# Optimization experiments

Hardware: AMD Instinct MI355X
Metric: run time of the kernel (lower is better)

Reference implementation:

```python
import jax, jax.numpy as jnp
import numpy as np

B, NB, DIM = 4096, 64, 256
CNT_R = 500
CNT_E = CNT_R * 2  # padding relation id == CNT_E maps to the masked row
N_WR = CNT_R * 2 + 1
N_ZQ = CNT_R * 2


def setup_inputs() -> dict:
    key = jax.random.key(0)
    ks = jax.random.split(key, 10)
    batch_nei_rid = jax.random.randint(ks[0], (B, NB), 0, N_WR, dtype=jnp.int64 if jax.config.read('jax_enable_x64') else jnp.int32)
    batch_nei_e_emb = jax.random.normal(ks[1], (B, NB, DIM), dtype=jnp.float32)
    batch_nei_rw = jax.random.uniform(ks[2], (B, NB), dtype=jnp.float32)
    batch_q_rid = jax.random.randint(ks[3], (B,), 0, N_ZQ, dtype=jnp.int32)
    # xavier-normal-ish params
    def xav(k, shape):
        fan_in, fan_out = shape[-1], shape[-2] if len(shape) > 1 else shape[-1]
        std = (2.0 / (fan_in + fan_out)) ** 0.5
        return (jax.random.normal(k, shape) * std).astype(jnp.float32)
    w_r_weight = xav(ks[4], (N_WR, DIM))
    zq_weight = xav(ks[5], (N_ZQ, DIM))
    attn_W_w = xav(ks[6], (2 * DIM, 2 * DIM))   # [out, in], torch Linear layout
    attn_W_b = jnp.zeros((2 * DIM,), jnp.float32)
    u_a_w = xav(ks[7], (1, 2 * DIM))
    u_a_b = jnp.zeros((1,), jnp.float32)
    return {
        'batch_nei_rid': batch_nei_rid,
        'batch_nei_e_emb': batch_nei_e_emb,
        'batch_nei_rw': batch_nei_rw,
        'batch_q_rid': batch_q_rid,
        'w_r_weight': w_r_weight,
        'zq_weight': zq_weight,
        'attn_W_w': attn_W_w,
        'attn_W_b': attn_W_b,
        'u_a_w': u_a_w,
        'u_a_b': u_a_b,
    }


def reference(batch_nei_rid, batch_nei_e_emb, batch_nei_rw, batch_q_rid,
              w_r_weight, zq_weight, attn_W_w, attn_W_b, u_a_w, u_a_b):
    # relation hyperplane gather + TransH-style projection
    w_r = w_r_weight[batch_nei_rid]                                   # [B,NB,D]
    nrm = jnp.maximum(jnp.linalg.norm(w_r, axis=-1, keepdims=True), 1e-12)
    wn = w_r / nrm                                                    # f.normalize(p=2)
    e_tr = batch_nei_e_emb - jnp.sum(batch_nei_e_emb * wn, axis=-1, keepdims=True) * wn
    # mask_emb: 1 for real rows, 0 for padding row (index CNT_E)
    mask = (batch_nei_rid < CNT_E).astype(e_tr.dtype)[..., None]
    e_tr = e_tr * mask
    # nn attention: concat(z_q, e_Tr) -> Linear -> tanh -> Linear(1)
    z_q = zq_weight[batch_q_rid][:, None, :]                          # [B,1,D]
    cat = jnp.concatenate([jnp.broadcast_to(z_q, e_tr.shape), e_tr], axis=-1)  # [B,NB,2D]
    h = jnp.tanh(jnp.einsum('bni,oi->bno', cat, attn_W_w) + attn_W_b)
    _alpha = jnp.einsum('bni,oi->bno', h, u_a_w)[..., 0] + u_a_b[0]   # [B,NB]
    # mask_weight: 1e19 at padding row, subtracted before softmax
    _alpha = _alpha - jnp.where(batch_nei_rid == CNT_E, jnp.asarray(1e19, _alpha.dtype), jnp.asarray(0.0, _alpha.dtype))
    alpha = jax.nn.softmax(_alpha, axis=-1)
    attn = alpha + batch_nei_rw                                       # use_logic_attention
    return jnp.sum(attn[..., None] * e_tr, axis=-2)                   # [B,D]
```

## Files before the change

kernel.cpp:

```cpp
#include <hip/hip_runtime.h>
#include <math.h>

#define NB    64
#define DIM   256
#define TWOD  512
#define CNTE  1000
#define E2S   264
#define NQ    1000

typedef __attribute__((ext_vector_type(8))) short short8;
typedef __attribute__((ext_vector_type(4))) float f32x4;

union U16x8 { uint4 u; short8 s; };

__device__ __forceinline__ unsigned short f2bf(float x) {
    unsigned int u = __float_as_uint(x);
    u += 0x7fffu + ((u >> 16) & 1u);
    return (unsigned short)(u >> 16);
}
__device__ __forceinline__ float bf2f(unsigned short h) {
    return __uint_as_float(((unsigned int)h) << 16);
}

__global__ __launch_bounds__(128) void zpre_kernel(
    const float* __restrict__ zq_w, const float* __restrict__ attn_W,
    const float* __restrict__ attn_b, float* __restrict__ zpre)
{
    __shared__ float zq[8][DIM];
    const int t  = threadIdx.x;
    const int q0 = blockIdx.x * 8;
    const int o  = blockIdx.y * 128 + t;
    #pragma unroll
    for (int r = 0; r < 8; ++r) {
        zq[r][t]       = zq_w[(size_t)(q0 + r) * DIM + t];
        zq[r][t + 128] = zq_w[(size_t)(q0 + r) * DIM + t + 128];
    }
    __syncthreads();
    const float4* wrow = (const float4*)(attn_W + (size_t)o * TWOD);
    float acc[8];
    #pragma unroll
    for (int r = 0; r < 8; ++r) acc[r] = 0.f;
    #pragma unroll 8
    for (int kk = 0; kk < 64; ++kk) {
        float4 w = wrow[kk];
        #pragma unroll
        for (int r = 0; r < 8; ++r)
            acc[r] += w.x * zq[r][kk * 4 + 0] + w.y * zq[r][kk * 4 + 1]
                    + w.z * zq[r][kk * 4 + 2] + w.w * zq[r][kk * 4 + 3];
    }
    const float bo = attn_b[o];
    #pragma unroll
    for (int r = 0; r < 8; ++r)
        zpre[(size_t)(q0 + r) * TWOD + o] = acc[r] + bo;
}

__global__ __launch_bounds__(256) void pack_w_kernel(
    const float* __restrict__ attn_W, unsigned short* __restrict__ wbf)
{
    int f = blockIdx.x * 256 + threadIdx.x;
    int j    = f & 7;
    int lane = (f >> 3) & 63;
    int kt   = (f >> 9) & 7;
    int ot   = f >> 12;
    int o  = ot * 16 + (lane & 15);
    int ke = kt * 32 + (lane >> 4) * 8 + j;
    wbf[f] = f2bf(attn_W[(size_t)o * TWOD + 256 + ke]);
}

__global__ __launch_bounds__(256, 4) void encoder_attn_kernel(
    const int*   __restrict__ nei_rid,
    const float* __restrict__ nei_e,
    const float* __restrict__ nei_rw,
    const int*   __restrict__ q_rid,
    const float* __restrict__ w_r,
    const float* __restrict__ zq_w,
    const float* __restrict__ attn_W,
    const float* __restrict__ attn_b,
    const float* __restrict__ u_a_w,
    const float* __restrict__ zpre,
    const unsigned short* __restrict__ wbf,
    float*       __restrict__ out,
    int has_zpre)
{
    __shared__ __align__(16) unsigned short e2[NB * E2S];
    __shared__ float2 zu[TWOD];
    __shared__ __align__(16) float red_a[256];
    __shared__ float  pen[NB];
    __shared__ float  attn_lds[NB];

    const int b = blockIdx.x;
    const int t = threadIdx.x;
    const int qr = q_rid[b];

    if (has_zpre) {
        zu[t]       = make_float2(zpre[(size_t)qr * TWOD + t],       u_a_w[t]);
        zu[t + 256] = make_float2(zpre[(size_t)qr * TWOD + t + 256], u_a_w[t + 256]);
    } else {
        red_a[t] = zq_w[(size_t)qr * DIM + t];
        __syncthreads();
        float a0 = 0.f, a1 = 0.f;
        const float4* w0 = (const float4*)(attn_W + (size_t)t * TWOD);
        const float4* w1 = (const float4*)(attn_W + (size_t)(t + 256) * TWOD);
        const float4* zz = (const float4*)red_a;
        #pragma unroll 8
        for (int kk = 0; kk < 64; ++kk) {
            float4 z = zz[kk], u0 = w0[kk], u1 = w1[kk];
            a0 += u0.x * z.x + u0.y * z.y + u0.z * z.z + u0.w * z.w;
            a1 += u1.x * z.x + u1.y * z.y + u1.z * z.z + u1.w * z.w;
        }
        zu[t]       = make_float2(a0 + attn_b[t],       u_a_w[t]);
        zu[t + 256] = make_float2(a1 + attn_b[t + 256], u_a_w[t + 256]);
        __syncthreads();
    }

    {
        const int q = t & 7;
        #pragma unroll 1
        for (int half = 0; half < 2; ++half) {
            const int n = (t >> 3) + half * 32;
            const int rid = nei_rid[b * NB + n];
            const float4* e4 = (const float4*)(nei_e + ((size_t)(b * NB + n)) * DIM) + q * 8;
            const float4* w4 = (const float4*)(w_r + (size_t)rid * DIM) + q * 8;
            float4 ev[8], wv[8];
            float sew = 0.f, sww = 0.f;
            #pragma unroll
            for (int j = 0; j < 8; ++j) {
                ev[j] = e4[j]; wv[j] = w4[j];
                sew += ev[j].x * wv[j].x + ev[j].y * wv[j].y + ev[j].z * wv[j].z + ev[j].w * wv[j].w;
                sww += wv[j].x * wv[j].x + wv[j].y * wv[j].y + wv[j].z * wv[j].z + wv[j].w * wv[j].w;
            }
            sew += __shfl_xor(sew, 1); sew += __shfl_xor(sew, 2); sew += __shfl_xor(sew, 4);
            sww += __shfl_xor(sww, 1); sww += __shfl_xor(sww, 2); sww += __shfl_xor(sww, 4);
            float nc   = fmaxf(sqrtf(sww), 1e-12f);
            float coef = sew / (nc * nc);
            float maskf = (rid < CNTE) ? 1.f : 0.f;
            if (q == 0) pen[n] = (rid == CNTE) ? 1e19f : 0.f;
            unsigned short* e2row = e2 + n * E2S + q * 32;
            #pragma unroll
            for (int jj = 0; jj < 4; ++jj) {
                float4 e0 = ev[jj * 2],     w0 = wv[jj * 2];
                float4 e1 = ev[jj * 2 + 1], w1 = wv[jj * 2 + 1];
                uint4 pk;
                pk.x = (unsigned int)f2bf((e0.x - coef * w0.x) * maskf)
                     | ((unsigned int)f2bf((e0.y - coef * w0.y) * maskf) << 16);
                pk.y = (unsigned int)f2bf((e0.z - coef * w0.z) * maskf)
                     | ((unsigned int)f2bf((e0.w - coef * w0.w) * maskf) << 16);
                pk.z = (unsigned int)f2bf((e1.x - coef * w1.x) * maskf)
                     | ((unsigned int)f2bf((e1.y - coef * w1.y) * maskf) << 16);
                pk.w = (unsigned int)f2bf((e1.z - coef * w1.z) * maskf)
                     | ((unsigned int)f2bf((e1.w - coef * w1.w) * maskf) << 16);
                *(uint4*)(e2row + jj * 8) = pk;
            }
        }
    }
    __syncthreads();

    const int wv_id = t >> 6;
    const int lane  = t & 63;
    const int l15 = lane & 15, lq = lane >> 4;
    const uint4* wbase = (const uint4*)wbf + (size_t)(wv_id * 8) * 512 + lane;

    #pragma unroll 1
    for (int mh = 0; mh < 2; ++mh) {
        short8 af[2][8];
        #pragma unroll
        for (int mt = 0; mt < 2; ++mt)
            #pragma unroll
            for (int kt = 0; kt < 8; ++kt) {
                U16x8 u;
                u.u = *(const uint4*)(e2 + ((mh * 2 + mt) * 16 + l15) * E2S + kt * 32 + lq * 8);
                af[mt][kt] = u.s;
            }

        f32x4 lpv[2];
        lpv[0] = (f32x4){0.f, 0.f, 0.f, 0.f};
        lpv[1] = (f32x4){0.f, 0.f, 0.f, 0.f};

        #pragma unroll 1
        for (int ot = 0; ot < 8; ++ot) {
            uint4 bb[8];
            #pragma unroll
            for (int kt = 0; kt < 8; ++kt) bb[kt] = wbase[ot * 512 + kt * 64];

            const int otg = wv_id * 8 + ot;
            const float2 zub = zu[otg * 16 + l15];
            f32x4 acc[2];
            acc[0] = (f32x4){zub.x, zub.x, zub.x, zub.x};
            acc[1] = acc[0];

            #pragma unroll
            for (int kt = 0; kt < 8; ++kt) {
                U16x8 u; u.u = bb[kt];
                acc[0] = __builtin_amdgcn_mfma_f32_16x16x32_bf16(af[0][kt], u.s, acc[0], 0, 0, 0);
                acc[1] = __builtin_amdgcn_mfma_f32_16x16x32_bf16(af[1][kt], u.s, acc[1], 0, 0, 0);
            }

            const float uy2 = -2.0f * zub.y;
            #pragma unroll
            for (int mt = 0; mt < 2; ++mt)
                #pragma unroll
                for (int r = 0; r < 4; ++r) {
                    float x = acc[mt][r];
                    float e = __expf(x + x);
                    lpv[mt][r] += uy2 * __builtin_amdgcn_rcpf(e + 1.0f);
                }
        }

        #pragma unroll
        for (int mt = 0; mt < 2; ++mt)
            #pragma unroll
            for (int r = 0; r < 4; ++r) {
                float v = lpv[mt][r];
                v += __shfl_xor(v, 1); v += __shfl_xor(v, 2);
                v += __shfl_xor(v, 4); v += __shfl_xor(v, 8);
                if (l15 == 0)
                    red_a[wv_id * 64 + (mh * 2 + mt) * 16 + lq * 4 + r] = v;
            }
    }
    __syncthreads();

    if (t < NB) {
        float lgt = red_a[t] + red_a[64 + t] + red_a[128 + t] + red_a[192 + t]
                  - pen[t];
        float m = lgt;
        #pragma unroll
        for (int off = 32; off > 0; off >>= 1) m = fmaxf(m, __shfl_xor(m, off));
        float ex = __expf(lgt - m);
        float s = ex;
        #pragma unroll
        for (int off = 32; off > 0; off >>= 1) s += __shfl_xor(s, off);
        attn_lds[t] = ex / s + nei_rw[b * NB + t];
    }
    __syncthreads();

    float oacc = 0.f;
    #pragma unroll 8
    for (int nn = 0; nn < NB; ++nn)
        oacc += attn_lds[nn] * bf2f(e2[nn * E2S + t]);
    out[(size_t)b * DIM + t] = oacc;
}

extern "C" void kernel_launch(void* const* d_in, const int* in_sizes, int n_in,
                              void* d_out, int out_size, void* d_ws, size_t ws_size,
                              hipStream_t stream) {
    const int*   nei_rid = (const int*)  d_in[0];
    const float* nei_e   = (const float*)d_in[1];
    const float* nei_rw  = (const float*)d_in[2];
    const int*   q_rid   = (const int*)  d_in[3];
    const float* w_r     = (const float*)d_in[4];
    const float* zq_w    = (const float*)d_in[5];
    const float* attn_W  = (const float*)d_in[6];
    const float* attn_b  = (const float*)d_in[7];
    const float* u_a_w   = (const float*)d_in[8];

    float* out = (float*)d_out;
    const int B = in_sizes[3];

    const size_t ZPRE_BYTES = (size_t)NQ * TWOD * 4;
    const size_t WBF_BYTES  = (size_t)512 * 256 * 2;
    const int has_zpre = (ws_size >= ZPRE_BYTES + WBF_BYTES) ? 1 : 0;

    float*          zpre = (float*)d_ws;
    unsigned short* wbf  = has_zpre
        ? (unsigned short*)((char*)d_ws + ZPRE_BYTES)
        : (unsigned short*)d_ws;

    if (has_zpre)
        hipLaunchKernelGGL(zpre_kernel, dim3(NQ / 8, 4), dim3(128), 0, stream,
                           zq_w, attn_W, attn_b, zpre);
    hipLaunchKernelGGL(pack_w_kernel, dim3(512), dim3(256), 0, stream, attn_W, wbf);
    hipLaunchKernelGGL(encoder_attn_kernel, dim3(B), dim3(256), 0, stream,
                       nei_rid, nei_e, nei_rw, q_rid, w_r, zq_w, attn_W, attn_b,
                       u_a_w, zpre, wbf, out, has_zpre);
}
```

Baseline: 502.4 us.

## Prefetch next weight tile, use packed bf16 convert, hoist rid loads

Software-pipelines the global loads of the bf16 weight fragments so the next output tile's B operands are fetched while the current MFMAs and the tanh epilogue run. It also replaces the manual round-to-nearest bf16 conversion with the hardware v_cvt_pk_bf16_f32 instruction, and the mask multiply with a bitmask AND. The norm-and-divide becomes a single reciprocal of the clamped squared norm. Both relation ids are loaded up front. The changes risk extra register pressure from the live prefetch buffer and slight rounding differences from the approximate reciprocal.

```diff
diff --git a/kernel.cpp b/kernel.cpp
--- a/kernel.cpp
+++ b/kernel.cpp
@@ -20,6 +20,11 @@
 }
 __device__ __forceinline__ float bf2f(unsigned short h) {
     return __uint_as_float(((unsigned int)h) << 16);
+}
+__device__ __forceinline__ unsigned int cvt_pk_bf16(float a, float b) {
+    unsigned int r;
+    asm("v_cvt_pk_bf16_f32 %0, %1, %2" : "=v"(r) : "v"(a), "v"(b));
+    return r;
 }
 
 __global__ __launch_bounds__(128) void zpre_kernel(
@@ -114,11 +119,14 @@
     }
 
     {
-        const int q = t & 7;
+        const int q  = t & 7;
+        const int n0 = t >> 3;
+        const int rid0 = nei_rid[b * NB + n0];
+        const int rid1 = nei_rid[b * NB + n0 + 32];
         #pragma unroll 1
         for (int half = 0; half < 2; ++half) {
-            const int n = (t >> 3) + half * 32;
-            const int rid = nei_rid[b * NB + n];
+            const int n   = n0 + half * 32;
+            const int rid = half ? rid1 : rid0;
             const float4* e4 = (const float4*)(nei_e + ((size_t)(b * NB + n)) * DIM) + q * 8;
             const float4* w4 = (const float4*)(w_r + (size_t)rid * DIM) + q * 8;
             float4 ev[8], wv[8];
@@ -131,9 +139,8 @@
             }
             sew += __shfl_xor(sew, 1); sew += __shfl_xor(sew, 2); sew += __shfl_xor(sew, 4);
             sww += __shfl_xor(sww, 1); sww += __shfl_xor(sww, 2); sww += __shfl_xor(sww, 4);
-            float nc   = fmaxf(sqrtf(sww), 1e-12f);
-            float coef = sew / (nc * nc);
-            float maskf = (rid < CNTE) ? 1.f : 0.f;
+            const float coef = sew * __builtin_amdgcn_rcpf(fmaxf(sww, 1e-24f));
+            const unsigned int mbits = (rid < CNTE) ? 0xFFFFFFFFu : 0u;
             if (q == 0) pen[n] = (rid == CNTE) ? 1e19f : 0.f;
             unsigned short* e2row = e2 + n * E2S + q * 32;
             #pragma unroll
@@ -141,14 +148,10 @@
                 float4 e0 = ev[jj * 2],     w0 = wv[jj * 2];
                 float4 e1 = ev[jj * 2 + 1], w1 = wv[jj * 2 + 1];
                 uint4 pk;
-                pk.x = (unsigned int)f2bf((e0.x - coef * w0.x) * maskf)
-                     | ((unsigned int)f2bf((e0.y - coef * w0.y) * maskf) << 16);
-                pk.y = (unsigned int)f2bf((e0.z - coef * w0.z) * maskf)
-                     | ((unsigned int)f2bf((e0.w - coef * w0.w) * maskf) << 16);
-                pk.z = (unsigned int)f2bf((e1.x - coef * w1.x) * maskf)
-                     | ((unsigned int)f2bf((e1.y - coef * w1.y) * maskf) << 16);
-                pk.w = (unsigned int)f2bf((e1.z - coef * w1.z) * maskf)
-                     | ((unsigned int)f2bf((e1.w - coef * w1.w) * maskf) << 16);
+                pk.x = cvt_pk_bf16(fmaf(-coef, w0.x, e0.x), fmaf(-coef, w0.y, e0.y)) & mbits;
+                pk.y = cvt_pk_bf16(fmaf(-coef, w0.z, e0.z), fmaf(-coef, w0.w, e0.w)) & mbits;
+                pk.z = cvt_pk_bf16(fmaf(-coef, w1.x, e1.x), fmaf(-coef, w1.y, e1.y)) & mbits;
+                pk.w = cvt_pk_bf16(fmaf(-coef, w1.z, e1.z), fmaf(-coef, w1.w, e1.w)) & mbits;
                 *(uint4*)(e2row + jj * 8) = pk;
             }
         }
@@ -160,6 +163,10 @@
     const int l15 = lane & 15, lq = lane >> 4;
     const uint4* wbase = (const uint4*)wbf + (size_t)(wv_id * 8) * 512 + lane;
 
+    uint4 bb[8];
+    #pragma unroll
+    for (int kt = 0; kt < 8; ++kt) bb[kt] = wbase[kt * 64];
+
     #pragma unroll 1
     for (int mh = 0; mh < 2; ++mh) {
         short8 af[2][8];
@@ -178,10 +185,6 @@
 
         #pragma unroll 1
         for (int ot = 0; ot < 8; ++ot) {
-            uint4 bb[8];
-            #pragma unroll
-            for (int kt = 0; kt < 8; ++kt) bb[kt] = wbase[ot * 512 + kt * 64];
-
             const int otg = wv_id * 8 + ot;
             const float2 zub = zu[otg * 16 + l15];
             f32x4 acc[2];
@@ -194,6 +197,10 @@
                 acc[0] = __builtin_amdgcn_mfma_f32_16x16x32_bf16(af[0][kt], u.s, acc[0], 0, 0, 0);
                 acc[1] = __builtin_amdgcn_mfma_f32_16x16x32_bf16(af[1][kt], u.s, acc[1], 0, 0, 0);
             }
+
+            #pragma unroll
+            for (int kt = 0; kt < 8; ++kt)
+                bb[kt] = wbase[((ot + 1) & 7) * 512 + kt * 64];
 
             const float uy2 = -2.0f * zub.y;
             #pragma unroll
```

New measurement: 502.2 us. About the same (-0.0%).
